# Optimization experiments

Measured on AMD Instinct MI355X. Metric: run time of the kernel, lower is better.

Reference implementation:

```python
import jax, jax.numpy as jnp
import numpy as np
from jax import lax

B, CIN, COUT, H, W = 16, 128, 256, 56, 56
KH, KW = 3, 3
STRIDE = (1, 1)
PAD = ((1, 1), (1, 1))
DILATION = (1, 1)
GROUPS = 1


def setup_inputs() -> dict:
    key = jax.random.key(0)
    k1, k2, k3 = jax.random.split(key, 3)
    x = jax.random.normal(k1, (B, CIN, H, W), dtype=jnp.float32)
    weight = jax.random.normal(k2, (COUT, CIN // GROUPS, KH, KW), dtype=jnp.float32)
    bias = jax.random.normal(k3, (COUT,), dtype=jnp.float32)
    return {"x": x, "weight": weight, "bias": bias}


def reference(x, weight, bias):
    # Toeplitz matrix-vector product == grouped 2D convolution (cross-correlation)
    # with zero padding, plus per-output-channel bias.
    out = lax.conv_general_dilated(
        x, weight,
        window_strides=STRIDE,
        padding=PAD,
        rhs_dilation=DILATION,
        dimension_numbers=("NCHW", "OIHW", "NCHW"),
        feature_group_count=GROUPS,
    )
    return out + bias[None, :, None, None]
```

## Files before the change

kernel.cpp:

```cpp
#include <hip/hip_runtime.h>
#include <hip/hip_bf16.h>


#define XT_BYTES   15204352u
#define SLACK      8192u
#define WT_OFFSET  (XT_BYTES + SLACK)
#define WT_BYTES   589824u
#define WS_NEED    (WT_OFFSET + WT_BYTES)

typedef __bf16 bf16x8 __attribute__((ext_vector_type(8)));
typedef float  f32x4  __attribute__((ext_vector_type(4)));
typedef unsigned short ushort8v __attribute__((ext_vector_type(8)));

__device__ __forceinline__ unsigned short f2bf(float f) {
  unsigned u = __builtin_bit_cast(unsigned, f);
  u += 0x7fffu + ((u >> 16) & 1u);
  return (unsigned short)(u >> 16);
}

__device__ __forceinline__ void gll16(const void* g, const void* l) {
  __builtin_amdgcn_global_load_lds(
      (const __attribute__((address_space(1))) unsigned int*)g,
      (__attribute__((address_space(3))) unsigned int*)l, 16, 0, 0);
}

__global__ void prep(const float* __restrict__ x, const float* __restrict__ wsrc,
                     unsigned short* __restrict__ xt, unsigned short* __restrict__ wt) {
  int blk = blockIdx.x;
  int t = threadIdx.x;
  if (blk < 896) {
    __shared__ unsigned short tile[128][58];
    int b = blk / 56, h = blk % 56;
    int ci = t >> 1, half = t & 1;
    const float* src = x + ((size_t)(b * 128 + ci)) * 3136 + h * 56 + half * 28;
    #pragma unroll
    for (int q = 0; q < 7; ++q) {
      float4 v = *(const float4*)&src[q * 4];
      int wb = half * 28 + q * 4;
      tile[ci][wb + 0] = f2bf(v.x);
      tile[ci][wb + 1] = f2bf(v.y);
      tile[ci][wb + 2] = f2bf(v.z);
      tile[ci][wb + 3] = f2bf(v.w);
    }
    unsigned short* row = xt + (size_t)b * 475136 + (size_t)(h + 1) * 8192;
    if (t < 128) {
      int slot = t >> 4;
      int px = slot ? 56 + slot : 0;
      uint4 z; z.x = z.y = z.z = z.w = 0u;
      *(uint4*)(row + px * 128 + (t & 15) * 8) = z;
    }
    __syncthreads();
    if (t < 224) {
      int wo = t >> 2, chunk = t & 3;
      unsigned short* dst = row + (size_t)(wo + 1) * 128 + chunk * 32;
      #pragma unroll
      for (int q = 0; q < 4; ++q) {
        ushort8v v;
        #pragma unroll
        for (int j = 0; j < 8; ++j) v[j] = tile[chunk * 32 + q * 8 + j][wo];
        *(ushort8v*)&dst[q * 8] = v;
      }
    }
  } else if (blk < 928) {
    int idx = blk - 896;
    int b = idx >> 1, zr = (idx & 1) ? 57 : 0;
    uint4* dst = (uint4*)(xt + (size_t)b * 475136 + (size_t)zr * 8192);
    uint4 z; z.x = z.y = z.z = z.w = 0u;
    #pragma unroll
    for (int q = 0; q < 4; ++q) dst[t + q * 256] = z;
  } else {
    int kt = blk - 928;
    int tap = kt >> 1;
    int ci0 = (kt & 1) * 64;
    #pragma unroll
    for (int q = 0; q < 8; ++q) {
      int n2 = t + q * 256;
      int pm = n2 >> 10, n = n2 & 1023;
      int r = n >> 3;
      int co = pm * 128 + r;
      int kg = (n & 7) ^ (r & 7);
      const float* src = wsrc + (size_t)co * 1152 + (size_t)(ci0 + kg * 8) * 9 + tap;
      ushort8v v;
      #pragma unroll
      for (int j = 0; j < 8; ++j) v[j] = f2bf(src[j * 9]);
      *(ushort8v*)&wt[(size_t)kt * 16384 + pm * 8192 + n * 8] = v;
    }
  }
}


__global__ __launch_bounds__(256, 4) void conv_gemm(
    const unsigned short* __restrict__ xt,
    const char* __restrict__ wt,
    const float* __restrict__ bias,
    float* __restrict__ out) {
  __shared__ __align__(16) char lds[32768];

  int bid = blockIdx.x;
  int sw = (bid & 7) * 112 + (bid >> 3);
  int pm = sw & 1;
  int pn = sw >> 1;
  int bimg = pn / 28;
  int h0 = (pn - bimg * 28) * 2;

  int tid = threadIdx.x;
  int wv = tid >> 6, l = tid & 63;
  int wm = wv >> 1, wn = wv & 1;
  int lm = l & 15, lg = l >> 4, x7 = lm & 7;

  int aoff0 = wm * 8192 + lm * 128 + ((lg ^ x7) << 4);
  int boff0 = 16384 + wn * 8192 + lm * 128 + ((lg ^ x7) << 4);

  const char* aB = wt + pm * 16384 + wv * 4096 + l * 16;
  const unsigned short* bB[4];
  #pragma unroll
  for (int q = 0; q < 4; ++q) {
    int n = wv * 256 + q * 64 + l;
    int px = n >> 3;
    int kg = (n & 7) ^ (px & 7);
    bB[q] = xt + ((size_t)((bimg * 58 + h0 + (px >> 6)) * 64 + (px & 63))) * 128 + kg * 8;
  }

  f32x4 acc[4][4];
  #pragma unroll
  for (int m = 0; m < 4; ++m)
    #pragma unroll
    for (int n = 0; n < 4; ++n)
      acc[m][n] = (f32x4){0.f, 0.f, 0.f, 0.f};

  auto stage = [&](int kt) {
    int tap = kt >> 1;
    int kh = tap >= 6 ? 2 : (tap >= 3 ? 1 : 0);
    int kw = tap - kh * 3;
    int koff = (kh * 64 + kw) * 128 + (kt & 1) * 64;
    const char* sA = aB + kt * 32768;
    char* dA = &lds[wv * 4096];
    char* dB = &lds[16384 + wv * 4096];
    #pragma unroll
    for (int q = 0; q < 4; ++q) {
      gll16(sA + q * 1024, dA + q * 1024);
      gll16(bB[q] + koff, dB + q * 1024);
    }
  };

  for (int kt = 0; kt < 18; ++kt) {
    stage(kt);
    __syncthreads();
    bf16x8 a0[4], b0[4];
    #pragma unroll
    for (int m = 0; m < 4; ++m) a0[m] = *(const bf16x8*)(lds + aoff0 + m * 2048);
    #pragma unroll
    for (int n = 0; n < 4; ++n) b0[n] = *(const bf16x8*)(lds + boff0 + n * 2048);
    #pragma unroll
    for (int m = 0; m < 4; ++m)
      #pragma unroll
      for (int n = 0; n < 4; ++n)
        acc[m][n] = __builtin_amdgcn_mfma_f32_16x16x32_bf16(a0[m], b0[n], acc[m][n], 0, 0, 0);
    bf16x8 a1[4], b1[4];
    #pragma unroll
    for (int m = 0; m < 4; ++m) a1[m] = *(const bf16x8*)(lds + ((aoff0 ^ 64) + m * 2048));
    #pragma unroll
    for (int n = 0; n < 4; ++n) b1[n] = *(const bf16x8*)(lds + ((boff0 ^ 64) + n * 2048));
    #pragma unroll
    for (int m = 0; m < 4; ++m)
      #pragma unroll
      for (int n = 0; n < 4; ++n)
        acc[m][n] = __builtin_amdgcn_mfma_f32_16x16x32_bf16(a1[m], b1[n], acc[m][n], 0, 0, 0);
    if (kt < 17) __syncthreads();
  }

  #pragma unroll
  for (int m = 0; m < 4; ++m) {
    int co = pm * 128 + wm * 64 + m * 16 + lg * 4;
    f32x4 bb = *(const f32x4*)&bias[co];
    size_t obase = ((size_t)bimg * 256 + co) * 3136;
    #pragma unroll
    for (int n = 0; n < 4; ++n) {
      int px = wn * 64 + n * 16 + lm;
      int w_ = px & 63;
      int h_ = h0 + (px >> 6);
      if (w_ < 56) {
        float* o = out + obase + (size_t)h_ * 56 + w_;
        #pragma unroll
        for (int r = 0; r < 4; ++r)
          o[(size_t)r * 3136] = acc[m][n][r] + bb[r];
      }
    }
  }
}


__global__ void conv_naive(const float* __restrict__ x, const float* __restrict__ w,
                           const float* __restrict__ bias, float* __restrict__ out) {
  int idx = blockIdx.x * 256 + threadIdx.x;
  if (idx >= 16 * 256 * 56 * 56) return;
  int wo = idx % 56; int t = idx / 56;
  int ho = t % 56; t /= 56;
  int co = t % 256; int b = t / 256;
  float acc = bias[co];
  for (int ci = 0; ci < 128; ++ci) {
    const float* xp = x + ((size_t)(b * 128 + ci)) * 3136;
    const float* wp = w + ((size_t)(co * 128 + ci)) * 9;
    for (int kh = 0; kh < 3; ++kh) {
      int hi = ho + kh - 1;
      if (hi < 0 || hi >= 56) continue;
      for (int kw = 0; kw < 3; ++kw) {
        int wi = wo + kw - 1;
        if (wi < 0 || wi >= 56) continue;
        acc += xp[hi * 56 + wi] * wp[kh * 3 + kw];
      }
    }
  }
  out[idx] = acc;
}

extern "C" void kernel_launch(void* const* d_in, const int* in_sizes, int n_in,
                              void* d_out, int out_size, void* d_ws, size_t ws_size,
                              hipStream_t stream) {
  const float* x    = (const float*)d_in[0];
  const float* wgt  = (const float*)d_in[1];
  const float* bias = (const float*)d_in[2];
  float* out = (float*)d_out;

  if (ws_size < (size_t)WS_NEED) {
    conv_naive<<<(16 * 256 * 56 * 56 + 255) / 256, 256, 0, stream>>>(x, wgt, bias, out);
    return;
  }

  unsigned short* xt = (unsigned short*)d_ws;
  unsigned short* wt = (unsigned short*)((char*)d_ws + WT_OFFSET);

  prep<<<946, 256, 0, stream>>>(x, wgt, xt, wt);
  conv_gemm<<<896, 256, 0, stream>>>(xt, (const char*)wt, bias, out);
}
```

Before: 58.68 us.

## Double-buffer LDS with K=32 stages and repack weights to match

Cuts the GEMM K-step from 64 to 32 channels and splits the 32KB LDS into two buffers, so the next stage's global-to-LDS loads are issued while the current stage's MFMAs run. Only one barrier per iteration remains. The weight prep kernel and the LDS swizzle are changed to a 4-way XOR layout with 64-byte rows to fit the new tiling, and launch bounds are raised to 5 blocks per CU. In exchange it does twice as many iterations and barriers, and the tighter register budget from the higher occupancy target could cause spills.

```diff
diff --git a/kernel.cpp b/kernel.cpp
--- a/kernel.cpp
+++ b/kernel.cpp
@@ -69,27 +69,34 @@
     #pragma unroll
     for (int q = 0; q < 4; ++q) dst[t + q * 256] = z;
   } else {
-    int kt = blk - 928;
-    int tap = kt >> 1;
-    int ci0 = (kt & 1) * 64;
-    #pragma unroll
-    for (int q = 0; q < 8; ++q) {
-      int n2 = t + q * 256;
-      int pm = n2 >> 10, n = n2 & 1023;
-      int r = n >> 3;
-      int co = pm * 128 + r;
-      int kg = (n & 7) ^ (r & 7);
-      const float* src = wsrc + (size_t)co * 1152 + (size_t)(ci0 + kg * 8) * 9 + tap;
-      ushort8v v;
+    int k64 = blk - 928;
+    int tap = k64 >> 1;
+    int ci_base = (k64 & 1) * 64;
+    #pragma unroll
+    for (int h = 0; h < 2; ++h) {
+      int kt = k64 * 2 + h;
+      int ci0 = ci_base + h * 32;
       #pragma unroll
-      for (int j = 0; j < 8; ++j) v[j] = f2bf(src[j * 9]);
-      *(ushort8v*)&wt[(size_t)kt * 16384 + pm * 8192 + n * 8] = v;
-    }
-  }
-}
-
-
-__global__ __launch_bounds__(256, 4) void conv_gemm(
+      for (int pm = 0; pm < 2; ++pm) {
+        #pragma unroll
+        for (int q = 0; q < 2; ++q) {
+          int n = t + q * 256;
+          int r = n >> 2, s = n & 3;
+          int kg = s ^ (r & 3);
+          int co = pm * 128 + r;
+          const float* src = wsrc + (size_t)co * 1152 + (size_t)(ci0 + kg * 8) * 9 + tap;
+          ushort8v v;
+          #pragma unroll
+          for (int j = 0; j < 8; ++j) v[j] = f2bf(src[j * 9]);
+          *(ushort8v*)&wt[((size_t)kt * 2 + pm) * 4096 + n * 8] = v;
+        }
+      }
+    }
+  }
+}
+
+
+__global__ __launch_bounds__(256, 5) void conv_gemm(
     const unsigned short* __restrict__ xt,
     const char* __restrict__ wt,
     const float* __restrict__ bias,
@@ -106,19 +113,20 @@
   int tid = threadIdx.x;
   int wv = tid >> 6, l = tid & 63;
   int wm = wv >> 1, wn = wv & 1;
-  int lm = l & 15, lg = l >> 4, x7 = lm & 7;
-
-  int aoff0 = wm * 8192 + lm * 128 + ((lg ^ x7) << 4);
-  int boff0 = 16384 + wn * 8192 + lm * 128 + ((lg ^ x7) << 4);
-
-  const char* aB = wt + pm * 16384 + wv * 4096 + l * 16;
-  const unsigned short* bB[4];
+  int lm = l & 15, lg = l >> 4;
+  int swz = ((lg ^ (lm & 3)) << 4);
+
+  int aoff0 = wm * 4096 + lm * 64 + swz;
+  int boff0 = 8192 + wn * 4096 + lm * 64 + swz;
+
+  const char* aB = wt + pm * 8192 + (wv * 64 + l) * 16;
+  const unsigned short* bB[2];
   #pragma unroll
-  for (int q = 0; q < 4; ++q) {
-    int n = wv * 256 + q * 64 + l;
-    int px = n >> 3;
-    int kg = (n & 7) ^ (px & 7);
-    bB[q] = xt + ((size_t)((bimg * 58 + h0 + (px >> 6)) * 64 + (px & 63))) * 128 + kg * 8;
+  for (int j = 0; j < 2; ++j) {
+    int n = wv * 64 + l + j * 256;
+    int px = n >> 2;
+    int kg = (n & 3) ^ (px & 3);
+    bB[j] = xt + ((size_t)((bimg * 58 + h0 + (px >> 6)) * 64 + (px & 63))) * 128 + kg * 8;
   }
 
   f32x4 acc[4][4];
@@ -128,45 +136,37 @@
     for (int n = 0; n < 4; ++n)
       acc[m][n] = (f32x4){0.f, 0.f, 0.f, 0.f};
 
-  auto stage = [&](int kt) {
-    int tap = kt >> 1;
+  auto stage = [&](int kt, int buf) {
+    int tap = kt >> 2;
     int kh = tap >= 6 ? 2 : (tap >= 3 ? 1 : 0);
     int kw = tap - kh * 3;
-    int koff = (kh * 64 + kw) * 128 + (kt & 1) * 64;
-    const char* sA = aB + kt * 32768;
-    char* dA = &lds[wv * 4096];
-    char* dB = &lds[16384 + wv * 4096];
-    #pragma unroll
-    for (int q = 0; q < 4; ++q) {
-      gll16(sA + q * 1024, dA + q * 1024);
-      gll16(bB[q] + koff, dB + q * 1024);
-    }
+    int koff = (kh * 64 + kw) * 128 + (kt & 3) * 32;
+    const char* sA = aB + kt * 16384;
+    char* dA = &lds[buf * 16384 + (wv * 64 + l) * 16];
+    char* dB = dA + 8192;
+    gll16(sA, dA);
+    gll16(sA + 4096, dA + 4096);
+    gll16(bB[0] + koff, dB);
+    gll16(bB[1] + koff, dB + 4096);
   };
 
-  for (int kt = 0; kt < 18; ++kt) {
-    stage(kt);
-    __syncthreads();
-    bf16x8 a0[4], b0[4];
-    #pragma unroll
-    for (int m = 0; m < 4; ++m) a0[m] = *(const bf16x8*)(lds + aoff0 + m * 2048);
-    #pragma unroll
-    for (int n = 0; n < 4; ++n) b0[n] = *(const bf16x8*)(lds + boff0 + n * 2048);
+  stage(0, 0);
+  __syncthreads();
+
+  for (int kt = 0; kt < 36; ++kt) {
+    const char* base = &lds[(kt & 1) * 16384];
+    if (kt < 35) stage(kt + 1, (kt + 1) & 1);
+    bf16x8 a[4], b[4];
+    #pragma unroll
+    for (int m = 0; m < 4; ++m) a[m] = *(const bf16x8*)(base + aoff0 + m * 1024);
+    #pragma unroll
+    for (int n = 0; n < 4; ++n) b[n] = *(const bf16x8*)(base + boff0 + n * 1024);
     #pragma unroll
     for (int m = 0; m < 4; ++m)
       #pragma unroll
       for (int n = 0; n < 4; ++n)
-        acc[m][n] = __builtin_amdgcn_mfma_f32_16x16x32_bf16(a0[m], b0[n], acc[m][n], 0, 0, 0);
-    bf16x8 a1[4], b1[4];
-    #pragma unroll
-    for (int m = 0; m < 4; ++m) a1[m] = *(const bf16x8*)(lds + ((aoff0 ^ 64) + m * 2048));
-    #pragma unroll
-    for (int n = 0; n < 4; ++n) b1[n] = *(const bf16x8*)(lds + ((boff0 ^ 64) + n * 2048));
-    #pragma unroll
-    for (int m = 0; m < 4; ++m)
-      #pragma unroll
-      for (int n = 0; n < 4; ++n)
-        acc[m][n] = __builtin_amdgcn_mfma_f32_16x16x32_bf16(a1[m], b1[n], acc[m][n], 0, 0, 0);
-    if (kt < 17) __syncthreads();
+        acc[m][n] = __builtin_amdgcn_mfma_f32_16x16x32_bf16(a[m], b[n], acc[m][n], 0, 0, 0);
+    if (kt < 35) __syncthreads();
   }
 
   #pragma unroll
```

New measurement: 63.45 us. 1.08x slower.
